# Kernel tuning notes

Measured on AMD Instinct MI355X. Metric: run time of the kernel, lower is better.

Reference implementation:

```python
import jax, jax.numpy as jnp
import numpy as np

NUM_VARS = 512
HIDDEN = 16
TOPK = 8
TEMP = 1.0


def setup_inputs() -> dict:
    key = jax.random.key(0)
    ks = jax.random.split(key, 6)
    B, L, N, H = 8, 4096, NUM_VARS, HIDDEN
    x = jax.random.normal(ks[0], (B, L, N), dtype=jnp.float32)
    # learned params (xavier-ish scale)
    var_embed = jax.random.normal(ks[1], (N, H), dtype=jnp.float32) * (1.0 / np.sqrt(H))
    Wq = jax.random.normal(ks[2], (H, H), dtype=jnp.float32) * (1.0 / np.sqrt(H))
    bq = jnp.zeros((H,), dtype=jnp.float32)
    Wk = jax.random.normal(ks[3], (H, H), dtype=jnp.float32) * (1.0 / np.sqrt(H))
    bk = jnp.zeros((H,), dtype=jnp.float32)
    return {"x": x, "var_embed": var_embed, "Wq": Wq, "bq": bq, "Wk": Wk, "bk": bk}


def reference(x, var_embed, Wq, bq, Wk, bk):
    # x: [B, L, N]; var_embed: [N, H]
    # Eval-mode path (no Gumbel noise). sim is identical across batch in the
    # original (var_embed is expanded), so compute it once: [N, N].
    Q = var_embed @ Wq.T + bq                      # [N, H]
    K = var_embed @ Wk.T + bk                      # [N, H]
    sim = Q @ K.T                                  # [N, N]
    N = sim.shape[0]
    sim = jnp.where(jnp.eye(N, dtype=bool), jnp.float32(-1e9), sim)
    vals, idx = jax.lax.top_k(sim, TOPK)           # [N, k]
    w = jax.nn.softmax(vals / TEMP, axis=-1)       # [N, k]
    gathered = x[:, :, idx]                        # [B, L, N, k] irregular gather
    return jnp.einsum('blnk,nk->bln', gathered, w)  # [B, L, N]
```

## Files before the change

### kernel.cpp

```cpp
#include <hip/hip_runtime.h>
#include <hip/hip_bf16.h>
#include <math.h>

#define NVARS 512
#define HID   16
#define TOPK  8

__global__ __launch_bounds__(512) void routing_kernel(
    const float* __restrict__ ve,
    const float* __restrict__ Wq,
    const float* __restrict__ bq,
    const float* __restrict__ Wk,
    const float* __restrict__ bk,
    int*   __restrict__ out_idx,
    float* __restrict__ out_w)
{
    __shared__ float Ks[NVARS][HID + 1];

    const int t    = threadIdx.x;
    const int wave = t >> 6;
    const int lane = t & 63;
    const int n    = blockIdx.x * 8 + wave;

    float vrow[HID];
    #pragma unroll
    for (int j = 0; j < HID; ++j) vrow[j] = ve[t * HID + j];
    #pragma unroll
    for (int h = 0; h < HID; ++h) {
        float s = bk[h];
        #pragma unroll
        for (int j = 0; j < HID; ++j) s += vrow[j] * Wk[h * HID + j];
        Ks[t][h] = s;
    }

    float q[HID];
    #pragma unroll
    for (int j = 0; j < HID; ++j) vrow[j] = ve[n * HID + j];
    #pragma unroll
    for (int h = 0; h < HID; ++h) {
        float s = bq[h];
        #pragma unroll
        for (int j = 0; j < HID; ++j) s += vrow[j] * Wq[h * HID + j];
        q[h] = s;
    }

    __syncthreads();

    float vals[8];
    #pragma unroll
    for (int i = 0; i < 8; ++i) {
        const int m = i * 64 + lane;
        float s = 0.f;
        #pragma unroll
        for (int h = 0; h < HID; ++h) s += q[h] * Ks[m][h];
        vals[i] = (m == n) ? -1.0e9f : s;
    }

    float mx = 0.f, my_val = 0.f, sum_exp = 0.f;
    int my_idx = 0;
    #pragma unroll
    for (int r = 0; r < TOPK; ++r) {
        float bv = vals[0];
        int   bi = lane;
        #pragma unroll
        for (int i = 1; i < 8; ++i) {
            const int m = i * 64 + lane;
            if (vals[i] > bv) { bv = vals[i]; bi = m; }
        }
        #pragma unroll
        for (int off = 32; off >= 1; off >>= 1) {
            const float ov = __shfl_xor(bv, off);
            const int   oi = __shfl_xor(bi, off);
            if (ov > bv || (ov == bv && oi < bi)) { bv = ov; bi = oi; }
        }
        if (r == 0) mx = bv;
        sum_exp += __expf(bv - mx);
        if (lane == r) { my_val = bv; my_idx = bi; }
        if ((bi & 63) == lane) {
            const int slot = bi >> 6;
            #pragma unroll
            for (int i = 0; i < 8; ++i)
                if (slot == i) vals[i] = -3.4e38f;
        }
    }

    if (lane < TOPK) {
        out_idx[n * TOPK + lane] = my_idx;
        out_w[n * TOPK + lane]   = __expf(my_val - mx) / sum_exp;
    }
}

__global__ __launch_bounds__(512) void apply_kernel(
    const float* __restrict__ x,
    const int*   __restrict__ gidx,
    const float* __restrict__ gw,
    float*       __restrict__ out)
{
    __shared__ float xs[4 * NVARS];

    const int t = threadIdx.x;
    const int4   i0 = ((const int4*)gidx)[2 * t + 0];
    const int4   i1 = ((const int4*)gidx)[2 * t + 1];
    const float4 w0 = ((const float4*)gw)[2 * t + 0];
    const float4 w1 = ((const float4*)gw)[2 * t + 1];

    const long base = (long)blockIdx.x * 32;

    #pragma unroll 1
    for (int g = 0; g < 32; g += 4) {
        const float4 v = ((const float4*)(x + (base + g) * NVARS))[t];
        __syncthreads();
        ((float4*)xs)[t] = v;
        __syncthreads();

        #pragma unroll
        for (int r = 0; r < 4; ++r) {
            const float* xr = xs + r * NVARS;
            float acc = xr[i0.x] * w0.x + xr[i0.y] * w0.y
                      + xr[i0.z] * w0.z + xr[i0.w] * w0.w
                      + xr[i1.x] * w1.x + xr[i1.y] * w1.y
                      + xr[i1.z] * w1.z + xr[i1.w] * w1.w;
            out[(base + g + r) * NVARS + t] = acc;
        }
    }
}

extern "C" void kernel_launch(void* const* d_in, const int* in_sizes, int n_in,
                              void* d_out, int out_size, void* d_ws, size_t ws_size,
                              hipStream_t stream) {
    const float* x  = (const float*)d_in[0];
    const float* ve = (const float*)d_in[1];
    const float* Wq = (const float*)d_in[2];
    const float* bq = (const float*)d_in[3];
    const float* Wk = (const float*)d_in[4];
    const float* bk = (const float*)d_in[5];
    float* out = (float*)d_out;

    int*   idx_ws = (int*)d_ws;
    float* w_ws   = (float*)((char*)d_ws + NVARS * TOPK * sizeof(int));

    routing_kernel<<<64, 512, 0, stream>>>(ve, Wq, bq, Wk, bk, idx_ws, w_ws);
    apply_kernel<<<1024, 512, 0, stream>>>(x, idx_ws, w_ws, out);
}
```

Before: 144.0 us.

## Double-buffer apply tile in interleaved float4 LDS layout with register prefetch

The apply kernel now stores four rows of x interleaved per variable as float4 in shared memory, so each gathered index fetches all four rows in one 16-byte LDS read instead of four scalar reads. Global loads for the next group of rows are issued into registers before the current group is computed, and two LDS buffers alternate, which overlaps memory latency with compute. Each thread now does four strided scalar global loads per group instead of one float4 load, which may hurt coalescing. Shared memory use doubles.

Measured after the change: 138.9 us (median of 2 runs). 3.5% less time.

```diff
diff --git a/kernel.cpp b/kernel.cpp
--- a/kernel.cpp
+++ b/kernel.cpp
@@ -96,7 +96,7 @@
     const float* __restrict__ gw,
     float*       __restrict__ out)
 {
-    __shared__ float xs[4 * NVARS];
+    __shared__ float4 xs[2][NVARS];
 
     const int t = threadIdx.x;
     const int4   i0 = ((const int4*)gidx)[2 * t + 0];
@@ -106,22 +106,44 @@
 
     const long base = (long)blockIdx.x * 32;
 
+    const float* xp = x + base * NVARS + t;
+    float v0 = xp[0 * NVARS];
+    float v1 = xp[1 * NVARS];
+    float v2 = xp[2 * NVARS];
+    float v3 = xp[3 * NVARS];
+
     #pragma unroll 1
-    for (int g = 0; g < 32; g += 4) {
-        const float4 v = ((const float4*)(x + (base + g) * NVARS))[t];
-        __syncthreads();
-        ((float4*)xs)[t] = v;
+    for (int g = 0; g < 8; ++g) {
+        float4* buf = xs[g & 1];
+        buf[t] = make_float4(v0, v1, v2, v3);
         __syncthreads();
 
-        #pragma unroll
-        for (int r = 0; r < 4; ++r) {
-            const float* xr = xs + r * NVARS;
-            float acc = xr[i0.x] * w0.x + xr[i0.y] * w0.y
-                      + xr[i0.z] * w0.z + xr[i0.w] * w0.w
-                      + xr[i1.x] * w1.x + xr[i1.y] * w1.y
-                      + xr[i1.z] * w1.z + xr[i1.w] * w1.w;
-            out[(base + g + r) * NVARS + t] = acc;
+        if (g < 7) {
+            const float* xn = x + (base + 4 * (g + 1)) * NVARS + t;
+            v0 = xn[0 * NVARS];
+            v1 = xn[1 * NVARS];
+            v2 = xn[2 * NVARS];
+            v3 = xn[3 * NVARS];
         }
+
+        float ax = 0.f, ay = 0.f, az = 0.f, aw = 0.f;
+        float4 c;
+        c = buf[i0.x]; ax += c.x * w0.x; ay += c.y * w0.x; az += c.z * w0.x; aw += c.w * w0.x;
+        c = buf[i0.y]; ax += c.x * w0.y; ay += c.y * w0.y; az += c.z * w0.y; aw += c.w * w0.y;
+        c = buf[i0.z]; ax += c.x * w0.z; ay += c.y * w0.z; az += c.z * w0.z; aw += c.w * w0.z;
+        c = buf[i0.w]; ax += c.x * w0.w; ay += c.y * w0.w; az += c.z * w0.w; aw += c.w * w0.w;
+        c = buf[i1.x]; ax += c.x * w1.x; ay += c.y * w1.x; az += c.z * w1.x; aw += c.w * w1.x;
+        c = buf[i1.y]; ax += c.x * w1.y; ay += c.y * w1.y; az += c.z * w1.y; aw += c.w * w1.y;
+        c = buf[i1.z]; ax += c.x * w1.z; ay += c.y * w1.z; az += c.z * w1.z; aw += c.w * w1.z;
+        c = buf[i1.w]; ax += c.x * w1.w; ay += c.y * w1.w; az += c.z * w1.w; aw += c.w * w1.w;
+
+        float* o = out + (base + 4 * g) * NVARS + t;
+        o[0 * NVARS] = ax;
+        o[1 * NVARS] = ay;
+        o[2 * NVARS] = az;
+        o[3 * NVARS] = aw;
+
+        __syncthreads();
     }
 }
 
```

## Interleave four rows per wave in LDS as float4 and drop block barriers

Applied to the files above, without the earlier changes.

The apply kernel now gives each wave its own four rows of x, stored transposed in shared memory as float4 per column. One LDS gather then serves four output rows at once. The block-wide __syncthreads loop is removed and the launch becomes 2048 blocks of 256 threads. The aim is fewer LDS gather instructions and no barriers. In exchange, global loads and stores become scalar per row rather than float4, and the index and weight tables are reloaded for each column group.

Measured after the change: 145.1 us. Within noise of the previous version (+0.8%).

```diff
diff --git a/kernel.cpp b/kernel.cpp
--- a/kernel.cpp
+++ b/kernel.cpp
@@ -90,38 +90,59 @@
     }
 }
 
-__global__ __launch_bounds__(512) void apply_kernel(
+__global__ __launch_bounds__(256) void apply_kernel(
     const float* __restrict__ x,
     const int*   __restrict__ gidx,
     const float* __restrict__ gw,
     float*       __restrict__ out)
 {
-    __shared__ float xs[4 * NVARS];
+    __shared__ float4 xs[4][NVARS];
 
-    const int t = threadIdx.x;
-    const int4   i0 = ((const int4*)gidx)[2 * t + 0];
-    const int4   i1 = ((const int4*)gidx)[2 * t + 1];
-    const float4 w0 = ((const float4*)gw)[2 * t + 0];
-    const float4 w1 = ((const float4*)gw)[2 * t + 1];
+    const int t    = threadIdx.x;
+    const int wave = t >> 6;
+    const int lane = t & 63;
+    float4* buf = xs[wave];
 
-    const long base = (long)blockIdx.x * 32;
+    const long row0 = (long)blockIdx.x * 16 + wave * 4;
+    const float* xp = x + row0 * NVARS;
 
-    #pragma unroll 1
-    for (int g = 0; g < 32; g += 4) {
-        const float4 v = ((const float4*)(x + (base + g) * NVARS))[t];
-        __syncthreads();
-        ((float4*)xs)[t] = v;
-        __syncthreads();
+    float4 v[8];
+    #pragma unroll
+    for (int i = 0; i < 8; ++i) {
+        const int c = i * 64 + lane;
+        v[i].x = xp[0 * NVARS + c];
+        v[i].y = xp[1 * NVARS + c];
+        v[i].z = xp[2 * NVARS + c];
+        v[i].w = xp[3 * NVARS + c];
+    }
+    #pragma unroll
+    for (int i = 0; i < 8; ++i)
+        buf[i * 64 + lane] = v[i];
 
-        #pragma unroll
-        for (int r = 0; r < 4; ++r) {
-            const float* xr = xs + r * NVARS;
-            float acc = xr[i0.x] * w0.x + xr[i0.y] * w0.y
-                      + xr[i0.z] * w0.z + xr[i0.w] * w0.w
-                      + xr[i1.x] * w1.x + xr[i1.y] * w1.y
-                      + xr[i1.z] * w1.z + xr[i1.w] * w1.w;
-            out[(base + g + r) * NVARS + t] = acc;
-        }
+    #pragma unroll
+    for (int i = 0; i < 8; ++i) {
+        const int c = i * 64 + lane;
+        const int4   i0 = ((const int4*)gidx)[2 * c + 0];
+        const int4   i1 = ((const int4*)gidx)[2 * c + 1];
+        const float4 w0 = ((const float4*)gw)[2 * c + 0];
+        const float4 w1 = ((const float4*)gw)[2 * c + 1];
+
+        float ax = 0.f, ay = 0.f, az = 0.f, aw = 0.f;
+        float4 g;
+        g = buf[i0.x]; ax += g.x * w0.x; ay += g.y * w0.x; az += g.z * w0.x; aw += g.w * w0.x;
+        g = buf[i0.y]; ax += g.x * w0.y; ay += g.y * w0.y; az += g.z * w0.y; aw += g.w * w0.y;
+        g = buf[i0.z]; ax += g.x * w0.z; ay += g.y * w0.z; az += g.z * w0.z; aw += g.w * w0.z;
+        g = buf[i0.w]; ax += g.x * w0.w; ay += g.y * w0.w; az += g.z * w0.w; aw += g.w * w0.w;
+        g = buf[i1.x]; ax += g.x * w1.x; ay += g.y * w1.x; az += g.z * w1.x; aw += g.w * w1.x;
+        g = buf[i1.y]; ax += g.x * w1.y; ay += g.y * w1.y; az += g.z * w1.y; aw += g.w * w1.y;
+        g = buf[i1.z]; ax += g.x * w1.z; ay += g.y * w1.z; az += g.z * w1.z; aw += g.w * w1.z;
+        g = buf[i1.w]; ax += g.x * w1.w; ay += g.y * w1.w; az += g.z * w1.w; aw += g.w * w1.w;
+
+        float* o = out + row0 * NVARS + c;
+        o[0 * NVARS] = ax;
+        o[1 * NVARS] = ay;
+        o[2 * NVARS] = az;
+        o[3 * NVARS] = aw;
     }
 }
 
@@ -140,5 +161,5 @@
     float* w_ws   = (float*)((char*)d_ws + NVARS * TOPK * sizeof(int));
 
     routing_kernel<<<64, 512, 0, stream>>>(ve, Wq, bq, Wk, bk, idx_ws, w_ws);
-    apply_kernel<<<1024, 512, 0, stream>>>(x, idx_ws, w_ws, out);
+    apply_kernel<<<2048, 256, 0, stream>>>(x, idx_ws, w_ws, out);
 }
```
